# Optimization experiments

Hardware: AMD Instinct MI355X
Metric: run time of the kernel (lower is better)

## Reference

```python
import jax, jax.numpy as jnp
import numpy as np

B, S, D = 4, 2048, 1024   # batch, seq_len, d_model
H, DK, DV = 16, 64, 64    # heads, key_size, head_size
NEG_BIG = 1e12


def setup_inputs() -> dict:
    key = jax.random.key(0)
    ks = jax.random.split(key, 11)
    s = 0.02  # weight scale
    return {
        "q": jax.random.normal(ks[0], (B, S, D), jnp.float32),
        "k": jax.random.normal(ks[1], (B, S, D), jnp.float32),
        "v": jax.random.normal(ks[2], (B, S, D), jnp.float32),
        "q_mask": jnp.ones((B, S), jnp.int32),
        "v_mask": jnp.ones((B, S), jnp.int32),
        "Wq": jax.random.normal(ks[3], (D, H * DK), jnp.float32) * s,
        "bq": jnp.zeros((H * DK,), jnp.float32),
        "Wk": jax.random.normal(ks[4], (D, H * DK), jnp.float32) * s,
        "bk": jnp.zeros((H * DK,), jnp.float32),
        "Wv": jax.random.normal(ks[5], (D, H * DV), jnp.float32) * s,
        "bv": jnp.zeros((H * DV,), jnp.float32),
        "Wo": jax.random.normal(ks[6], (H * DV, H * DV), jnp.float32) * s,
        "bo": jnp.zeros((H * DV,), jnp.float32),
    }


def reference(q, k, v, q_mask, v_mask, Wq, bq, Wk, bk, Wv, bv, Wo, bo):
    Bq, Sq, _ = q.shape
    Sk = k.shape[1]
    # projections -> (B, S, H, d)
    qw = (q @ Wq + bq).reshape(Bq, Sq, H, DK)
    kw = (k @ Wk + bk).reshape(Bq, Sk, H, DK)
    vw = (v @ Wv + bv).reshape(Bq, Sk, H, DV)
    # scores: (B, H, Sq, Sk)
    a = jnp.einsum('bjhd,bkhd->bhjk', qw, kw) / jnp.asarray(DK, qw.dtype) ** 0.5
    # v_mask: additive -inf-style masking on key axis (mode=1, axis=-1)
    vm = v_mask.astype(a.dtype)[:, None, None, :]
    a = a - (1.0 - vm) * NEG_BIG
    # a_mask = 'history_only' causal mask
    causal = jnp.tril(jnp.ones((Sq, Sk), a.dtype))
    a = a - (1.0 - causal) * NEG_BIG
    a = jax.nn.softmax(a, axis=-1)
    # attention output: (B, Sq, H, DV) -> (B, Sq, H*DV)
    o = jnp.einsum('bhjk,bkhd->bjhd', a, vw).reshape(Bq, Sq, H * DV)
    o = o @ Wo + bo
    # q_mask: multiplicative zeroing of padded query rows (mode=0)
    o = o * q_mask.astype(o.dtype)[:, :, None]
    return o
```

## Files before the change

### kernel.cpp

```cpp
#include <hip/hip_runtime.h>
#include <hip/hip_bf16.h>

#define Bb 4
#define Ss 2048
#define Dm 1024
#define Hh 16
#define DKk 64
#define DVv 64

using short8  = __attribute__((ext_vector_type(8))) short;
using short4v = __attribute__((ext_vector_type(4))) short;
using floatx4 = __attribute__((ext_vector_type(4))) float;

__device__ inline unsigned short f32_to_bf16(float f) {
    union { float f; unsigned int u; } x; x.f = f;
    unsigned int r = x.u + 0x7fffu + ((x.u >> 16) & 1u);
    return (unsigned short)(r >> 16);
}

__device__ inline unsigned int cvt_pk_bf16(float a, float b) {
    unsigned int r;
    asm("v_cvt_pk_bf16_f32 %0, %1, %2" : "=v"(r) : "v"(a), "v"(b));
    return r;
}

__device__ inline void dma16(const unsigned short* g, unsigned short* l) {
    __builtin_amdgcn_global_load_lds(
        (const __attribute__((address_space(1))) void*)g,
        (__attribute__((address_space(3))) void*)l, 16, 0, 0);
}

__global__ __launch_bounds__(256) void transpose_w4(
        const float* __restrict__ W0, const float* __restrict__ W1,
        const float* __restrict__ W2, const float* __restrict__ W3,
        unsigned short* __restrict__ T0, unsigned short* __restrict__ T1,
        unsigned short* __restrict__ T2, unsigned short* __restrict__ T3) {
    const float* W; unsigned short* Wt;
    switch (blockIdx.z) {
        case 0: W = W0; Wt = T0; break;
        case 1: W = W1; Wt = T1; break;
        case 2: W = W2; Wt = T2; break;
        default: W = W3; Wt = T3; break;
    }
    __shared__ float tile[32][33];
    int n0 = blockIdx.x * 32, k0 = blockIdx.y * 32;
    int tx = threadIdx.x, ty = threadIdx.y;
    #pragma unroll
    for (int i = 0; i < 32; i += 8)
        tile[ty + i][tx] = W[(size_t)(k0 + ty + i) * Dm + n0 + tx];
    __syncthreads();
    #pragma unroll
    for (int i = 0; i < 32; i += 8)
        Wt[(size_t)(n0 + ty + i) * Dm + k0 + tx] = f32_to_bf16(tile[tx][ty + i]);
}

__global__ __launch_bounds__(256) void cast_bf16(const float* __restrict__ X,
                                                 unsigned short* __restrict__ Y) {
    const int idx = blockIdx.x * 256 + threadIdx.x;
    const float4* x4 = (const float4*)X;
    float4 f0 = x4[idx * 2], f1 = x4[idx * 2 + 1];
    const float* p0 = (const float*)&f0;
    const float* p1 = (const float*)&f1;
    union { short8 v; unsigned short u[8]; } o;
    #pragma unroll
    for (int j = 0; j < 4; j++) {
        o.u[j]     = f32_to_bf16(p0[j]);
        o.u[4 + j] = f32_to_bf16(p1[j]);
    }
    *(short8*)(Y + (size_t)idx * 8) = o.v;
}

__global__ __launch_bounds__(256) void gemm_proj(const unsigned short* __restrict__ A,
                                                 const unsigned short* __restrict__ Bt,
                                                 const float* __restrict__ bias,
                                                 unsigned short* __restrict__ Out,
                                                 int mode) {
    const int wave = threadIdx.x >> 6;
    const int lane = threadIdx.x & 63;
    const int quad = lane >> 4;
    const int l16  = lane & 15;
    const int wr = wave & 1, wc = wave >> 1;
    const int m0 = blockIdx.x * 128;
    const int n0 = blockIdx.y * 128;

    __shared__ __align__(16) unsigned short Alds[4096];
    __shared__ __align__(16) unsigned short Blds[4096];

    const unsigned short* Asrc[2];
    const unsigned short* Bsrc[2];
    int Ldst[2];
    #pragma unroll
    for (int i = 0; i < 2; i++) {
        int L = (wave * 2 + i) * 64 + lane;
        int row = L >> 2, cpr = L & 3;
        int csrc = cpr ^ ((row >> 1) & 3);
        Ldst[i] = (wave * 2 + i) * 512;
        Asrc[i] = A  + (size_t)(m0 + row) * Dm + csrc * 8;
        Bsrc[i] = Bt + (size_t)(n0 + row) * Dm + csrc * 8;
    }

    int aoff[4], boff[4];
    #pragma unroll
    for (int r = 0; r < 4; r++) {
        int row = wr * 64 + r * 16 + l16;
        aoff[r] = row * 32 + (quad ^ ((row >> 1) & 3)) * 8;
        row = wc * 64 + r * 16 + l16;
        boff[r] = row * 32 + (quad ^ ((row >> 1) & 3)) * 8;
    }

    floatx4 acc[4][4] = {};

    for (int k0 = 0; k0 < Dm; k0 += 32) {
        __syncthreads();
        #pragma unroll
        for (int i = 0; i < 2; i++) {
            dma16(Asrc[i] + k0, &Alds[Ldst[i]]);
            dma16(Bsrc[i] + k0, &Blds[Ldst[i]]);
        }
        __syncthreads();

        short8 a[4], b[4];
        #pragma unroll
        for (int r = 0; r < 4; r++) a[r] = *(const short8*)(Alds + aoff[r]);
        #pragma unroll
        for (int c = 0; c < 4; c++) b[c] = *(const short8*)(Blds + boff[c]);
        #pragma unroll
        for (int r = 0; r < 4; r++)
            #pragma unroll
            for (int c = 0; c < 4; c++)
                acc[r][c] = __builtin_amdgcn_mfma_f32_16x16x32_bf16(a[r], b[c], acc[r][c], 0, 0, 0);
    }

    #pragma unroll
    for (int r = 0; r < 4; r++)
        #pragma unroll
        for (int c = 0; c < 4; c++) {
            int n = n0 + wc * 64 + c * 16 + l16;
            float bias_n = bias[n];
            int h = n >> 6, d = n & 63;
            #pragma unroll
            for (int i = 0; i < 4; i++) {
                int m = m0 + wr * 64 + r * 16 + quad * 4 + i;
                unsigned short ob = f32_to_bf16(acc[r][c][i] + bias_n);
                int bb = m >> 11, s = m & (Ss - 1);
                if (mode == 0)
                    Out[((size_t)(bb * Hh + h) * Ss + s) * 64 + d] = ob;
                else
                    Out[(((size_t)(bb * Hh + h) * 32 + (s >> 6)) * 64 + d) * 64 + (s & 63)] = ob;
            }
        }
}

__global__ __launch_bounds__(256) void gemm_final(const unsigned short* __restrict__ A,
                                                  const unsigned short* __restrict__ Bt,
                                                  const float* __restrict__ bias,
                                                  const int* __restrict__ q_mask,
                                                  float* __restrict__ Out) {
    const int wave = threadIdx.x >> 6;
    const int lane = threadIdx.x & 63;
    const int quad = lane >> 4;
    const int l16  = lane & 15;
    const int wr = wave & 1, wc = wave >> 1;
    const int m0 = blockIdx.x * 128;
    const int n0 = blockIdx.y * 128;

    __shared__ __align__(16) unsigned short Alds[4096];
    __shared__ __align__(16) unsigned short Blds[4096];

    const unsigned short* Asrc[2];
    const unsigned short* Bsrc[2];
    int Ldst[2];
    #pragma unroll
    for (int i = 0; i < 2; i++) {
        int L = (wave * 2 + i) * 64 + lane;
        int row = L >> 2, cpr = L & 3;
        int csrc = cpr ^ ((row >> 1) & 3);
        Ldst[i] = (wave * 2 + i) * 512;
        Asrc[i] = A  + (size_t)(m0 + row) * Dm + csrc * 8;
        Bsrc[i] = Bt + (size_t)(n0 + row) * Dm + csrc * 8;
    }

    int aoff[4], boff[4];
    #pragma unroll
    for (int r = 0; r < 4; r++) {
        int row = wr * 64 + r * 16 + l16;
        aoff[r] = row * 32 + (quad ^ ((row >> 1) & 3)) * 8;
        row = wc * 64 + r * 16 + l16;
        boff[r] = row * 32 + (quad ^ ((row >> 1) & 3)) * 8;
    }

    floatx4 acc[4][4] = {};

    for (int k0 = 0; k0 < Dm; k0 += 32) {
        __syncthreads();
        #pragma unroll
        for (int i = 0; i < 2; i++) {
            dma16(Asrc[i] + k0, &Alds[Ldst[i]]);
            dma16(Bsrc[i] + k0, &Blds[Ldst[i]]);
        }
        __syncthreads();

        short8 a[4], b[4];
        #pragma unroll
        for (int r = 0; r < 4; r++) a[r] = *(const short8*)(Alds + aoff[r]);
        #pragma unroll
        for (int c = 0; c < 4; c++) b[c] = *(const short8*)(Blds + boff[c]);
        #pragma unroll
        for (int r = 0; r < 4; r++)
            #pragma unroll
            for (int c = 0; c < 4; c++)
                acc[r][c] = __builtin_amdgcn_mfma_f32_16x16x32_bf16(a[r], b[c], acc[r][c], 0, 0, 0);
    }

    #pragma unroll
    for (int r = 0; r < 4; r++)
        #pragma unroll
        for (int c = 0; c < 4; c++) {
            int n = n0 + wc * 64 + c * 16 + l16;
            float bias_n = bias[n];
            #pragma unroll
            for (int i = 0; i < 4; i++) {
                int m = m0 + wr * 64 + r * 16 + quad * 4 + i;
                float qm = (float)q_mask[m];
                Out[(size_t)m * Dm + n] = (acc[r][c][i] + bias_n) * qm;
            }
        }
}

#define SCL 0.18033688f
#define PEN 1.44269504e12f

__global__ __launch_bounds__(512, 6) void attn_kernel(const unsigned short* __restrict__ Qp,
                                                      const unsigned short* __restrict__ Kp,
                                                      const unsigned short* __restrict__ Vt,
                                                      const int* __restrict__ v_mask,
                                                      unsigned short* __restrict__ AO) {
    const int wave = threadIdx.x >> 6;
    const int lane = threadIdx.x & 63;
    const int quad = lane >> 4;
    const int l16  = lane & 15;
    const int qi = (int)gridDim.x - 1 - (int)blockIdx.x;
    const int h  = blockIdx.y;
    const int b  = blockIdx.z;
    const int bh = b * Hh + h;
    const int qbase = qi * 128 + wave * 16;
    const int query = qbase + l16;

    __shared__ __align__(16) unsigned short Klds[2][4096];
    __shared__ __align__(16) unsigned short Vlds[2][4096];
    __shared__ int allv[32];

    {
        const int t = threadIdx.x;
        const int tile = t >> 4, sub = t & 15;
        const int4 vm = *(const int4*)(v_mask + b * Ss + tile * 64 + sub * 4);
        const bool ok = vm.x && vm.y && vm.z && vm.w;
        const unsigned long long bal = __ballot(ok);
        const int grp = tile & 3;
        if (sub == 0)
            allv[tile] = (int)(((bal >> (grp * 16)) & 0xFFFFull) == 0xFFFFull);
    }

    const int G    = threadIdx.x;
    const int grow = G >> 3, gc = G & 7;
    const int fS = (grow & 3) | ((grow >> 1) & 4);
    const int srcOff = grow * 64 + (gc ^ fS) * 8;
    const int ldsDst = wave * 512;

    const unsigned short* Kt_base = Kp + (size_t)bh * Ss * 64;
    const unsigned short* Vt_base = Vt + (size_t)bh * 32 * 4096;

    const unsigned short* qptr = Qp + ((size_t)bh * Ss + query) * 64 + quad * 8;
    const short8 qf0 = *(const short8*)(qptr);
    const short8 qf1 = *(const short8*)(qptr + 32);

    const int l3 = l16 & 3;
    const int fK = l3 | (((l16 >> 2) & 1) << 2);
    const int kslot = (quad ^ fK) * 8;
    int koff[4];
    #pragma unroll
    for (int kf = 0; kf < 4; kf++) {
        int row = (kf & 1) * 32 + ((l16 >> 2) << 3) + ((kf >> 1) << 2) + l3;
        koff[kf] = row * 64 + kslot;
    }
    const int fV = l3 | (((l16 >> 3) & 1) << 2);
    const int vslot = (quad ^ fV) * 8;
    int voff[4];
    #pragma unroll
    for (int f = 0; f < 4; f++) voff[f] = (f * 16 + l16) * 64 + vslot;

    floatx4 o[4] = {};
    float lrun = 0.f;

    const int diagw = 2 * qi + (wave >> 2);
    const int KT    = 2 * qi + 2;
    const int kbq   = quad * 8;

    dma16(Kt_base + srcOff, &Klds[0][ldsDst]);
    dma16(Vt_base + srcOff, &Vlds[0][ldsDst]);
    __syncthreads();

    int cur = 0;
    for (int kt = 0; kt < KT; kt++) {
        if (kt + 1 < KT) {
            const unsigned short* kn = Kt_base + (size_t)(kt + 1) * 4096;
            const unsigned short* vn = Vt_base + (size_t)(kt + 1) * 4096;
            dma16(kn + srcOff, &Klds[cur ^ 1][ldsDst]);
            dma16(vn + srcOff, &Vlds[cur ^ 1][ldsDst]);
        }

        if (kt <= diagw) {
            const unsigned short* Kc = &Klds[cur][0];
            const unsigned short* Vc = &Vlds[cur][0];
            const int kk = kt * 64;

            floatx4 st[4];
            #pragma unroll
            for (int kf = 0; kf < 4; kf++) {
                short8 a0 = *(const short8*)(Kc + koff[kf]);
                short8 a1 = *(const short8*)(Kc + (koff[kf] ^ 32));
                floatx4 t = {};
                t = __builtin_amdgcn_mfma_f32_16x16x32_bf16(a0, qf0, t, 0, 0, 0);
                t = __builtin_amdgcn_mfma_f32_16x16x32_bf16(a1, qf1, t, 0, 0, 0);
                st[kf] = t;
            }

            unsigned int pk[4][2];
            if ((kt == diagw) || (!allv[kt])) {
                #pragma unroll
                for (int kf = 0; kf < 4; kf++) {
                    const int kb = kk + (kf & 1) * 32 + kbq + ((kf >> 1) << 2);
                    const int4 vm = *(const int4*)(v_mask + b * Ss + kb);
                    const int vmi[4] = {vm.x, vm.y, vm.z, vm.w};
                    float p[4];
                    #pragma unroll
                    for (int i = 0; i < 4; i++) {
                        const int key = kb + i;
                        float pen = (vmi[i] == 0) ? PEN : 0.f;
                        if (key > query) pen += PEN;
                        p[i] = exp2f(fmaf(st[kf][i], SCL, -pen));
                        lrun += p[i];
                    }
                    pk[kf][0] = cvt_pk_bf16(p[0], p[1]);
                    pk[kf][1] = cvt_pk_bf16(p[2], p[3]);
                }
            } else {
                #pragma unroll
                for (int kf = 0; kf < 4; kf++) {
                    float p[4];
                    #pragma unroll
                    for (int i = 0; i < 4; i++) {
                        p[i] = exp2f(st[kf][i] * SCL);
                        lrun += p[i];
                    }
                    pk[kf][0] = cvt_pk_bf16(p[0], p[1]);
                    pk[kf][1] = cvt_pk_bf16(p[2], p[3]);
                }
            }

            union { short8 s; unsigned int u[4]; } pb0, pb1;
            pb0.u[0] = pk[0][0]; pb0.u[1] = pk[0][1];
            pb0.u[2] = pk[2][0]; pb0.u[3] = pk[2][1];
            pb1.u[0] = pk[1][0]; pb1.u[1] = pk[1][1];
            pb1.u[2] = pk[3][0]; pb1.u[3] = pk[3][1];

            #pragma unroll
            for (int f = 0; f < 4; f++) {
                short8 v0 = *(const short8*)(Vc + voff[f]);
                short8 v1 = *(const short8*)(Vc + (voff[f] ^ 32));
                o[f] = __builtin_amdgcn_mfma_f32_16x16x32_bf16(v0, pb0.s, o[f], 0, 0, 0);
                o[f] = __builtin_amdgcn_mfma_f32_16x16x32_bf16(v1, pb1.s, o[f], 0, 0, 0);
            }
        }

        __syncthreads();
        cur ^= 1;
    }

    lrun += __shfl_xor(lrun, 16, 64);
    lrun += __shfl_xor(lrun, 32, 64);
    const float ri = 1.0f / lrun;

    unsigned short* aop = AO + ((size_t)b * Ss + qbase + l16) * (Hh * DVv) + h * 64 + quad * 4;
    #pragma unroll
    for (int f = 0; f < 4; f++) {
        int2 w;
        w.x = (int)cvt_pk_bf16(o[f][0] * ri, o[f][1] * ri);
        w.y = (int)cvt_pk_bf16(o[f][2] * ri, o[f][3] * ri);
        *(int2*)(aop + f * 16) = w;
    }
}

extern "C" void kernel_launch(void* const* d_in, const int* in_sizes, int n_in,
                              void* d_out, int out_size, void* d_ws, size_t ws_size,
                              hipStream_t stream) {
    const float* q      = (const float*)d_in[0];
    const float* k      = (const float*)d_in[1];
    const float* v      = (const float*)d_in[2];
    const int*   q_mask = (const int*)d_in[3];
    const int*   v_mask = (const int*)d_in[4];
    const float* Wq     = (const float*)d_in[5];
    const float* bq     = (const float*)d_in[6];
    const float* Wk     = (const float*)d_in[7];
    const float* bk     = (const float*)d_in[8];
    const float* Wv     = (const float*)d_in[9];
    const float* bv     = (const float*)d_in[10];
    const float* Wo     = (const float*)d_in[11];
    const float* bo     = (const float*)d_in[12];
    float* out = (float*)d_out;

    char* ws = (char*)d_ws;
    const size_t WT_SZ = (size_t)Dm * Dm * 2;
    const size_t QP_SZ = (size_t)Bb * Hh * Ss * 64 * 2;
    unsigned short* Wtq = (unsigned short*)(ws);
    unsigned short* Wtk = (unsigned short*)(ws + WT_SZ);
    unsigned short* Wtv = (unsigned short*)(ws + 2 * WT_SZ);
    unsigned short* Wto = (unsigned short*)(ws + 3 * WT_SZ);
    unsigned short* Qp  = (unsigned short*)(ws + 4 * WT_SZ);
    unsigned short* Kp  = (unsigned short*)(ws + 4 * WT_SZ + QP_SZ);
    unsigned short* Vt  = (unsigned short*)(ws + 4 * WT_SZ + 2 * QP_SZ);
    unsigned short* AO  = (unsigned short*)(ws + 4 * WT_SZ + 3 * QP_SZ);

    hipLaunchKernelGGL(transpose_w4, dim3(Dm / 32, Dm / 32, 4), dim3(32, 8), 0, stream,
                       Wq, Wk, Wv, Wo, Wtq, Wtk, Wtv, Wto);

    const int M = Bb * Ss;
    const int castBlocks = M * Dm / (256 * 8);
    dim3 gg(M / 128, Dm / 128);

    hipLaunchKernelGGL(cast_bf16, dim3(castBlocks), dim3(256), 0, stream, q, AO);
    hipLaunchKernelGGL(gemm_proj, gg, dim3(256), 0, stream, AO, Wtq, bq, Qp, 0);
    hipLaunchKernelGGL(cast_bf16, dim3(castBlocks), dim3(256), 0, stream, k, AO);
    hipLaunchKernelGGL(gemm_proj, gg, dim3(256), 0, stream, AO, Wtk, bk, Kp, 0);
    hipLaunchKernelGGL(cast_bf16, dim3(castBlocks), dim3(256), 0, stream, v, AO);
    hipLaunchKernelGGL(gemm_proj, gg, dim3(256), 0, stream, AO, Wtv, bv, Vt, 1);

    dim3 ag(Ss / 128, Hh, Bb);
    hipLaunchKernelGGL(attn_kernel, ag, dim3(512), 0, stream, Qp, Kp, Vt, v_mask, AO);

    hipLaunchKernelGGL(gemm_final, gg, dim3(256), 0, stream, AO, Wto, bo, q_mask, out);
}
```

Before: 389.6 us.

## Pair causal query tiles per block and compute two row groups per wave

The attention kernel now runs 256-thread blocks, each handling two query tiles (qp and 15-qp) in sequence. This balances causal work across blocks and halves the grid. Each wave now covers 32 query rows instead of 16, so every K/V fragment read from LDS feeds twice as many MFMAs. The softmax row sum is computed with an MFMA against a ones vector instead of scalar adds and shuffles. In exchange, register pressure rises (launch bounds are now 256,2), fewer waves are resident, and the row sum is taken from bf16-rounded probabilities.

```diff
diff --git a/kernel.cpp b/kernel.cpp
--- a/kernel.cpp
+++ b/kernel.cpp
@@ -230,49 +230,48 @@
 #define SCL 0.18033688f
 #define PEN 1.44269504e12f
 
-__global__ __launch_bounds__(512, 6) void attn_kernel(const unsigned short* __restrict__ Qp,
+__global__ __launch_bounds__(256, 2) void attn_kernel(const unsigned short* __restrict__ Qp,
                                                       const unsigned short* __restrict__ Kp,
                                                       const unsigned short* __restrict__ Vt,
                                                       const int* __restrict__ v_mask,
                                                       unsigned short* __restrict__ AO) {
-    const int wave = threadIdx.x >> 6;
-    const int lane = threadIdx.x & 63;
+    const int tid  = threadIdx.x;
+    const int wave = tid >> 6;
+    const int lane = tid & 63;
     const int quad = lane >> 4;
     const int l16  = lane & 15;
-    const int qi = (int)gridDim.x - 1 - (int)blockIdx.x;
+    const int qp = blockIdx.x;
     const int h  = blockIdx.y;
     const int b  = blockIdx.z;
     const int bh = b * Hh + h;
-    const int qbase = qi * 128 + wave * 16;
-    const int query = qbase + l16;
 
     __shared__ __align__(16) unsigned short Klds[2][4096];
     __shared__ __align__(16) unsigned short Vlds[2][4096];
     __shared__ int allv[32];
 
     {
-        const int t = threadIdx.x;
-        const int tile = t >> 4, sub = t & 15;
-        const int4 vm = *(const int4*)(v_mask + b * Ss + tile * 64 + sub * 4);
-        const bool ok = vm.x && vm.y && vm.z && vm.w;
+        const int tile = tid >> 3, sub = tid & 7;
+        const int4 vmA = *(const int4*)(v_mask + b * Ss + tile * 64 + sub * 8);
+        const int4 vmB = *(const int4*)(v_mask + b * Ss + tile * 64 + sub * 8 + 4);
+        const bool ok = vmA.x && vmA.y && vmA.z && vmA.w &&
+                        vmB.x && vmB.y && vmB.z && vmB.w;
         const unsigned long long bal = __ballot(ok);
-        const int grp = tile & 3;
         if (sub == 0)
-            allv[tile] = (int)(((bal >> (grp * 16)) & 0xFFFFull) == 0xFFFFull);
-    }
-
-    const int G    = threadIdx.x;
-    const int grow = G >> 3, gc = G & 7;
-    const int fS = (grow & 3) | ((grow >> 1) & 4);
-    const int srcOff = grow * 64 + (gc ^ fS) * 8;
-    const int ldsDst = wave * 512;
-
+            allv[tile] = (int)(((bal >> ((tile & 7) * 8)) & 0xFFull) == 0xFFull);
+    }
+
+    int srcOff[2], ldsDst[2];
+    #pragma unroll
+    for (int i = 0; i < 2; i++) {
+        int G = i * 256 + tid;
+        int grow = G >> 3, gc = G & 7;
+        int fS = (grow & 3) | ((grow >> 1) & 4);
+        srcOff[i] = grow * 64 + (gc ^ fS) * 8;
+        ldsDst[i] = i * 2048 + wave * 512;
+    }
     const unsigned short* Kt_base = Kp + (size_t)bh * Ss * 64;
     const unsigned short* Vt_base = Vt + (size_t)bh * 32 * 4096;
-
-    const unsigned short* qptr = Qp + ((size_t)bh * Ss + query) * 64 + quad * 8;
-    const short8 qf0 = *(const short8*)(qptr);
-    const short8 qf1 = *(const short8*)(qptr + 32);
+    const int* vm_base = v_mask + b * Ss;
 
     const int l3 = l16 & 3;
     const int fK = l3 | (((l16 >> 2) & 1) << 2);
@@ -289,106 +288,152 @@
     #pragma unroll
     for (int f = 0; f < 4; f++) voff[f] = (f * 16 + l16) * 64 + vslot;
 
-    floatx4 o[4] = {};
-    float lrun = 0.f;
-
-    const int diagw = 2 * qi + (wave >> 2);
-    const int KT    = 2 * qi + 2;
-    const int kbq   = quad * 8;
-
-    dma16(Kt_base + srcOff, &Klds[0][ldsDst]);
-    dma16(Vt_base + srcOff, &Vlds[0][ldsDst]);
-    __syncthreads();
-
-    int cur = 0;
-    for (int kt = 0; kt < KT; kt++) {
-        if (kt + 1 < KT) {
-            const unsigned short* kn = Kt_base + (size_t)(kt + 1) * 4096;
-            const unsigned short* vn = Vt_base + (size_t)(kt + 1) * 4096;
-            dma16(kn + srcOff, &Klds[cur ^ 1][ldsDst]);
-            dma16(vn + srcOff, &Vlds[cur ^ 1][ldsDst]);
-        }
-
-        if (kt <= diagw) {
-            const unsigned short* Kc = &Klds[cur][0];
-            const unsigned short* Vc = &Vlds[cur][0];
-            const int kk = kt * 64;
-
-            floatx4 st[4];
-            #pragma unroll
-            for (int kf = 0; kf < 4; kf++) {
-                short8 a0 = *(const short8*)(Kc + koff[kf]);
-                short8 a1 = *(const short8*)(Kc + (koff[kf] ^ 32));
-                floatx4 t = {};
-                t = __builtin_amdgcn_mfma_f32_16x16x32_bf16(a0, qf0, t, 0, 0, 0);
-                t = __builtin_amdgcn_mfma_f32_16x16x32_bf16(a1, qf1, t, 0, 0, 0);
-                st[kf] = t;
+    short8 ones;
+    #pragma unroll
+    for (int i = 0; i < 8; i++) ones[i] = (short)0x3F80;
+
+    const int kbq = quad * 8;
+
+    auto run_phase = [&](int qi) {
+        const int qbase = qi * 128 + wave * 32;
+        const int q0 = qbase + l16;
+        const unsigned short* qptr = Qp + ((size_t)bh * Ss + q0) * 64 + quad * 8;
+        const short8 qf0 = *(const short8*)(qptr);
+        const short8 qf1 = *(const short8*)(qptr + 32);
+        const short8 qg0 = *(const short8*)(qptr + 16 * 64);
+        const short8 qg1 = *(const short8*)(qptr + 16 * 64 + 32);
+
+        floatx4 o0[4] = {}, o1[4] = {};
+        floatx4 sm0 = {}, sm1 = {};
+
+        const int diagw = 2 * qi + (wave >> 1);
+        const int KT    = 2 * qi + 2;
+
+        #pragma unroll
+        for (int i = 0; i < 2; i++) {
+            dma16(Kt_base + srcOff[i], &Klds[0][ldsDst[i]]);
+            dma16(Vt_base + srcOff[i], &Vlds[0][ldsDst[i]]);
+        }
+        __syncthreads();
+
+        int cur = 0;
+        for (int kt = 0; kt < KT; kt++) {
+            if (kt + 1 < KT) {
+                const unsigned short* kn = Kt_base + (size_t)(kt + 1) * 4096;
+                const unsigned short* vn = Vt_base + (size_t)(kt + 1) * 4096;
+                #pragma unroll
+                for (int i = 0; i < 2; i++) {
+                    dma16(kn + srcOff[i], &Klds[cur ^ 1][ldsDst[i]]);
+                    dma16(vn + srcOff[i], &Vlds[cur ^ 1][ldsDst[i]]);
+                }
             }
 
-            unsigned int pk[4][2];
-            if ((kt == diagw) || (!allv[kt])) {
+            if (kt <= diagw) {
+                const unsigned short* Kc = &Klds[cur][0];
+                const unsigned short* Vc = &Vlds[cur][0];
+                const int kk = kt * 64;
+
+                floatx4 st0[4], st1[4];
                 #pragma unroll
                 for (int kf = 0; kf < 4; kf++) {
-                    const int kb = kk + (kf & 1) * 32 + kbq + ((kf >> 1) << 2);
-                    const int4 vm = *(const int4*)(v_mask + b * Ss + kb);
-                    const int vmi[4] = {vm.x, vm.y, vm.z, vm.w};
-                    float p[4];
+                    short8 a0 = *(const short8*)(Kc + koff[kf]);
+                    short8 a1 = *(const short8*)(Kc + (koff[kf] ^ 32));
+                    floatx4 t = {};
+                    t = __builtin_amdgcn_mfma_f32_16x16x32_bf16(a0, qf0, t, 0, 0, 0);
+                    t = __builtin_amdgcn_mfma_f32_16x16x32_bf16(a1, qf1, t, 0, 0, 0);
+                    st0[kf] = t;
+                    floatx4 u = {};
+                    u = __builtin_amdgcn_mfma_f32_16x16x32_bf16(a0, qg0, u, 0, 0, 0);
+                    u = __builtin_amdgcn_mfma_f32_16x16x32_bf16(a1, qg1, u, 0, 0, 0);
+                    st1[kf] = u;
+                }
+
+                unsigned int pk0[4][2], pk1[4][2];
+                if ((kt == diagw) || (!allv[kt])) {
                     #pragma unroll
-                    for (int i = 0; i < 4; i++) {
-                        const int key = kb + i;
-                        float pen = (vmi[i] == 0) ? PEN : 0.f;
-                        if (key > query) pen += PEN;
-                        p[i] = exp2f(fmaf(st[kf][i], SCL, -pen));
-                        lrun += p[i];
+                    for (int kf = 0; kf < 4; kf++) {
+                        const int kb = kk + (kf & 1) * 32 + kbq + ((kf >> 1) << 2);
+                        const int4 vm = *(const int4*)(vm_base + kb);
+                        const int vmi[4] = {vm.x, vm.y, vm.z, vm.w};
+                        float p0[4], p1[4];
+                        #pragma unroll
+                        for (int i = 0; i < 4; i++) {
+                            const int key = kb + i;
+                            const float penm = (vmi[i] == 0) ? PEN : 0.f;
+                            const float pe0 = penm + ((key > q0) ? PEN : 0.f);
+                            const float pe1 = penm + ((key > q0 + 16) ? PEN : 0.f);
+                            p0[i] = exp2f(fmaf(st0[kf][i], SCL, -pe0));
+                            p1[i] = exp2f(fmaf(st1[kf][i], SCL, -pe1));
+                        }
+                        pk0[kf][0] = cvt_pk_bf16(p0[0], p0[1]);
+                        pk0[kf][1] = cvt_pk_bf16(p0[2], p0[3]);
+                        pk1[kf][0] = cvt_pk_bf16(p1[0], p1[1]);
+                        pk1[kf][1] = cvt_pk_bf16(p1[2], p1[3]);
                     }
-                    pk[kf][0] = cvt_pk_bf16(p[0], p[1]);
-                    pk[kf][1] = cvt_pk_bf16(p[2], p[3]);
+                } else {
+                    #pragma unroll
+                    for (int kf = 0; kf < 4; kf++) {
+                        float p0[4], p1[4];
+                        #pragma unroll
+                        for (int i = 0; i < 4; i++) {
+                            p0[i] = exp2f(st0[kf][i] * SCL);
+                            p1[i] = exp2f(st1[kf][i] * SCL);
+                        }
+                        pk0[kf][0] = cvt_pk_bf16(p0[0], p0[1]);
+                        pk0[kf][1] = cvt_pk_bf16(p0[2], p0[3]);
+                        pk1[kf][0] = cvt_pk_bf16(p1[0], p1[1]);
+                        pk1[kf][1] = cvt_pk_bf16(p1[2], p1[3]);
+                    }
                 }
-            } else {
+
+                union { short8 s; unsigned int u[4]; } pA0, pA1, pB0, pB1;
+                pA0.u[0] = pk0[0][0]; pA0.u[1] = pk0[0][1];
+                pA0.u[2] = pk0[2][0]; pA0.u[3] = pk0[2][1];
+                pA1.u[0] = pk0[1][0]; pA1.u[1] = pk0[1][1];
+                pA1.u[2] = pk0[3][0]; pA1.u[3] = pk0[3][1];
+                pB0.u[0] = pk1[0][0]; pB0.u[1] = pk1[0][1];
+                pB0.u[2] = pk1[2][0]; pB0.u[3] = pk1[2][1];
+                pB1.u[0] = pk1[1][0]; pB1.u[1] = pk1[1][1];
+                pB1.u[2] = pk1[3][0]; pB1.u[3] = pk1[3][1];
+
+                sm0 = __builtin_amdgcn_mfma_f32_16x16x32_bf16(ones, pA0.s, sm0, 0, 0, 0);
+                sm0 = __builtin_amdgcn_mfma_f32_16x16x32_bf16(ones, pA1.s, sm0, 0, 0, 0);
+                sm1 = __builtin_amdgcn_mfma_f32_16x16x32_bf16(ones, pB0.s, sm1, 0, 0, 0);
+                sm1 = __builtin_amdgcn_mfma_f32_16x16x32_bf16(ones, pB1.s, sm1, 0, 0, 0);
+
                 #pragma unroll
-                for (int kf = 0; kf < 4; kf++) {
-                    float p[4];
-                    #pragma unroll
-                    for (int i = 0; i < 4; i++) {
-                        p[i] = exp2f(st[kf][i] * SCL);
-                        lrun += p[i];
-                    }
-                    pk[kf][0] = cvt_pk_bf16(p[0], p[1]);
-                    pk[kf][1] = cvt_pk_bf16(p[2], p[3]);
+                for (int f = 0; f < 4; f++) {
+                    short8 v0 = *(const short8*)(Vc + voff[f]);
+                    short8 v1 = *(const short8*)(Vc + (voff[f] ^ 32));
+                    o0[f] = __builtin_amdgcn_mfma_f32_16x16x32_bf16(v0, pA0.s, o0[f], 0, 0, 0);
+                    o0[f] = __builtin_amdgcn_mfma_f32_16x16x32_bf16(v1, pA1.s, o0[f], 0, 0, 0);
+                    o1[f] = __builtin_amdgcn_mfma_f32_16x16x32_bf16(v0, pB0.s, o1[f], 0, 0, 0);
+                    o1[f] = __builtin_amdgcn_mfma_f32_16x16x32_bf16(v1, pB1.s, o1[f], 0, 0, 0);
                 }
             }
 
-            union { short8 s; unsigned int u[4]; } pb0, pb1;
-            pb0.u[0] = pk[0][0]; pb0.u[1] = pk[0][1];
-            pb0.u[2] = pk[2][0]; pb0.u[3] = pk[2][1];
-            pb1.u[0] = pk[1][0]; pb1.u[1] = pk[1][1];
-            pb1.u[2] = pk[3][0]; pb1.u[3] = pk[3][1];
-
-            #pragma unroll
-            for (int f = 0; f < 4; f++) {
-                short8 v0 = *(const short8*)(Vc + voff[f]);
-                short8 v1 = *(const short8*)(Vc + (voff[f] ^ 32));
-                o[f] = __builtin_amdgcn_mfma_f32_16x16x32_bf16(v0, pb0.s, o[f], 0, 0, 0);
-                o[f] = __builtin_amdgcn_mfma_f32_16x16x32_bf16(v1, pb1.s, o[f], 0, 0, 0);
-            }
-        }
-
-        __syncthreads();
-        cur ^= 1;
-    }
-
-    lrun += __shfl_xor(lrun, 16, 64);
-    lrun += __shfl_xor(lrun, 32, 64);
-    const float ri = 1.0f / lrun;
-
-    unsigned short* aop = AO + ((size_t)b * Ss + qbase + l16) * (Hh * DVv) + h * 64 + quad * 4;
-    #pragma unroll
-    for (int f = 0; f < 4; f++) {
-        int2 w;
-        w.x = (int)cvt_pk_bf16(o[f][0] * ri, o[f][1] * ri);
-        w.y = (int)cvt_pk_bf16(o[f][2] * ri, o[f][3] * ri);
-        *(int2*)(aop + f * 16) = w;
-    }
+            __syncthreads();
+            cur ^= 1;
+        }
+
+        const float ri0 = 1.0f / sm0[0];
+        const float ri1 = 1.0f / sm1[0];
+        unsigned short* aop0 = AO + ((size_t)b * Ss + q0) * (Hh * DVv) + h * 64 + quad * 4;
+        unsigned short* aop1 = aop0 + (size_t)16 * (Hh * DVv);
+        #pragma unroll
+        for (int f = 0; f < 4; f++) {
+            int2 w0, w1;
+            w0.x = (int)cvt_pk_bf16(o0[f][0] * ri0, o0[f][1] * ri0);
+            w0.y = (int)cvt_pk_bf16(o0[f][2] * ri0, o0[f][3] * ri0);
+            *(int2*)(aop0 + f * 16) = w0;
+            w1.x = (int)cvt_pk_bf16(o1[f][0] * ri1, o1[f][1] * ri1);
+            w1.y = (int)cvt_pk_bf16(o1[f][2] * ri1, o1[f][3] * ri1);
+            *(int2*)(aop1 + f * 16) = w1;
+        }
+    };
+
+    run_phase(15 - qp);
+    run_phase(qp);
 }
 
 extern "C" void kernel_launch(void* const* d_in, const int* in_sizes, int n_in,
@@ -435,8 +480,8 @@
     hipLaunchKernelGGL(cast_bf16, dim3(castBlocks), dim3(256), 0, stream, v, AO);
     hipLaunchKernelGGL(gemm_proj, gg, dim3(256), 0, stream, AO, Wtv, bv, Vt, 1);
 
-    dim3 ag(Ss / 128, Hh, Bb);
-    hipLaunchKernelGGL(attn_kernel, ag, dim3(512), 0, stream, Qp, Kp, Vt, v_mask, AO);
+    dim3 ag(Ss / 256, Hh, Bb);
+    hipLaunchKernelGGL(attn_kernel, ag, dim3(256), 0, stream, Qp, Kp, Vt, v_mask, AO);
 
     hipLaunchKernelGGL(gemm_final, gg, dim3(256), 0, stream, AO, Wto, bo, q_mask, out);
 }
```

Result: faster. 356.9 us (-8.4%).
